# Kernel optimization log

Measured on AMD Instinct MI355X. Metric: run time of the kernel, lower is better.

The kernel has to match this reference:

```python
import jax, jax.numpy as jnp
import numpy as np

B, N, C = 8, 4096, 512

def setup_inputs() -> dict:
    key = jax.random.key(0)
    k1, k2, k3, k4, k5, k6 = jax.random.split(key, 6)
    x = jax.random.normal(k1, (B, N, C), dtype=jnp.float32)
    adj = jax.random.uniform(k2, (B, C, C), dtype=jnp.float32)
    # params: stored [in, out] so y = x @ W + b (equivalent to torch Linear)
    s = 1.0 / np.sqrt(C)
    Wqkv = jax.random.uniform(k3, (C, 3 * C), dtype=jnp.float32, minval=-s, maxval=s)
    bqkv = jax.random.uniform(k4, (3 * C,), dtype=jnp.float32, minval=-s, maxval=s)
    Wo = jax.random.uniform(k5, (C, C), dtype=jnp.float32, minval=-s, maxval=s)
    bo = jax.random.uniform(k6, (C,), dtype=jnp.float32, minval=-s, maxval=s)
    return {"x": x, "adj": adj, "Wqkv": Wqkv, "bqkv": bqkv, "Wo": Wo, "bo": bo}

def reference(x, adj, Wqkv, bqkv, Wo, bo):
    # qkv projection + ReLU gating
    qkv = jnp.einsum('bnc,cd->bnd', x, Wqkv) + bqkv          # [B,N,3C]
    q, k, v = jnp.split(qkv, 3, axis=-1)                      # each [B,N,C]
    q, k, v = jax.nn.relu(q), jax.nn.relu(k), jax.nn.relu(v)
    dk = q.shape[-1]
    # channel-wise scores: q^T k over tokens -> [B,C,C]
    scores = jnp.einsum('bnc,bnd->bcd', q, k) / jnp.sqrt(jnp.float32(dk))
    attn = jax.nn.softmax(scores, axis=-1)
    attn = attn * adj                                         # post-softmax adjacency gate
    y = jnp.einsum('bnc,bcd->bnd', v, attn)                   # value.matmul(attention)
    return jnp.einsum('bnc,cd->bnd', y, Wo) + bo
```

## Files before the change

kernel.cpp:

```cpp
#include <hip/hip_runtime.h>

#define B_ 8
#define N_ 4096
#define C_ 512

typedef _Float16 f16;
typedef __attribute__((ext_vector_type(8))) _Float16 f16x8;
typedef __attribute__((ext_vector_type(4))) _Float16 f16x4;
typedef __attribute__((ext_vector_type(4))) float f32x4;

#define GLL16(gsrc, ldst)                                                      \
  __builtin_amdgcn_global_load_lds(                                            \
      (const __attribute__((address_space(1))) void*)(gsrc),                   \
      (__attribute__((address_space(3))) void*)(ldst), 16, 0, 0)

__device__ __forceinline__ int xcd_remap(int bid, int nwg) {
  return (bid & 7) * (nwg >> 3) + (bid >> 3);
}

template <int LDA2, int LDB2, int NT>
__device__ __forceinline__ void mainloop32(const char* __restrict__ Agb,
                                           const char* __restrict__ Bgb,
                                           f16* Als, f16* Bls,
                                           f32x4 (&acc)[4][4]) {
  const int tid = threadIdx.x;
  const int lane = tid & 63;
  const int wv = tid >> 6;
  const int wr = wv >> 1;
  const int wc = wv & 1;

  const int r15 = lane & 15;
  const int g8 = (lane >> 4) << 3;
  const int swz = (r15 & 3) << 3;
  const int kx = g8 ^ swz;
  const int awbase = (wr * 64 + r15) * 32;
  const int bwbase = (wc * 64 + r15) * 32;

  int rowl[2], colb[2];
#pragma unroll
  for (int ld = 0; ld < 2; ++ld) {
    const int doff = (ld * 256 + tid) * 16;
    rowl[ld] = doff >> 6;
    colb[ld] = (doff & 63) ^ ((rowl[ld] & 3) << 4);
  }

  auto stage = [&](int t) {
    if (t >= NT) return;
    f16* la = Als + (t & 1) * 4096 + wv * 512;
    f16* lb = Bls + (t & 1) * 4096 + wv * 512;
#pragma unroll
    for (int ld = 0; ld < 2; ++ld) {
      GLL16(Agb + (size_t)rowl[ld] * LDA2 + (size_t)t * 64 + colb[ld],
            la + ld * 2048);
      GLL16(Bgb + (size_t)rowl[ld] * LDB2 + (size_t)t * 64 + colb[ld],
            lb + ld * 2048);
    }
  };

  stage(0);
  __syncthreads();

  for (int T = 0; T < NT; ++T) {
    stage(T + 1);
    const f16* Ab = Als + (T & 1) * 4096;
    const f16* Bb = Bls + (T & 1) * 4096;
    f16x8 af[4], bf[4];
#pragma unroll
    for (int m = 0; m < 4; ++m)
      af[m] = *(const f16x8*)(Ab + awbase + m * 512 + kx);
#pragma unroll
    for (int n = 0; n < 4; ++n)
      bf[n] = *(const f16x8*)(Bb + bwbase + n * 512 + kx);
#pragma unroll
    for (int m = 0; m < 4; ++m)
#pragma unroll
      for (int n = 0; n < 4; ++n)
        acc[m][n] = __builtin_amdgcn_mfma_f32_16x16x32_f16(af[m], bf[n],
                                                           acc[m][n], 0, 0, 0);
    __syncthreads();
  }
}

#define ZERO_ACC(acc)                                                          \
  f32x4 acc[4][4];                                                             \
  _Pragma("unroll") for (int zi = 0; zi < 4; ++zi)                             \
      _Pragma("unroll") for (int zj = 0; zj < 4; ++zj) {                       \
    f32x4 z = {0.f, 0.f, 0.f, 0.f};                                            \
    acc[zi][zj] = z;                                                           \
  }

__global__ void __launch_bounds__(256) k_cvt_x(const float* __restrict__ in,
                                               f16* __restrict__ out) {
  const int i = blockIdx.x * 256 + threadIdx.x;
  float4 v = ((const float4*)in)[i];
  f16x4 h = {(f16)v.x, (f16)v.y, (f16)v.z, (f16)v.w};
  ((f16x4*)out)[i] = h;
}

__global__ void __launch_bounds__(256) k_transpose_w(const float* __restrict__ w,
                                                     f16* __restrict__ wt,
                                                     int cols) {
  const int idx = blockIdx.x * 256 + threadIdx.x;
  const int n = idx >> 9;
  const int c = idx & 511;
  wt[idx] = (f16)w[(size_t)c * cols + n];
}

__global__ void __launch_bounds__(256, 4)
    k_gemm_qkv(const f16* __restrict__ x16, const f16* __restrict__ wqkvt,
               const float* __restrict__ bqkv, f16* __restrict__ q_t,
               f16* __restrict__ k_t, f16* __restrict__ v16) {
  __shared__ alignas(16) f16 Als[2 * 4096];
  __shared__ alignas(16) f16 Bls[2 * 4096];
  const int l = xcd_remap(blockIdx.x, 3072);
  const int bx = l % 12;
  const int my = l / 12;
  const char* Agb = (const char*)(x16 + (size_t)my * 128 * C_);
  const char* Bgb = (const char*)(wqkvt + (size_t)bx * 128 * C_);
  ZERO_ACC(acc);
  mainloop32<C_ * 2, C_ * 2, C_ / 32>(Agb, Bgb, Als, Bls, acc);

  const int lane = threadIdx.x & 63, wv = threadIdx.x >> 6;
  const int wr = wv >> 1, wc = wv & 1;
  const int sec = bx >> 2;
  const int colbase = bx * 128 + wc * 64;
  const int rowbase = my * 128 + wr * 64;
  const int b = rowbase >> 12;
#pragma unroll
  for (int n = 0; n < 4; ++n) {
    const int col = colbase + n * 16 + (lane & 15);
    const int cch = col & 511;
    const float bias = bqkv[col];
#pragma unroll
    for (int m = 0; m < 4; ++m) {
      const int rg = rowbase + m * 16 + ((lane >> 4) << 2);
      const int nloc = rg & 4095;
      f32x4 a = acc[m][n];
      f16x4 h = {(f16)fmaxf(a[0] + bias, 0.f), (f16)fmaxf(a[1] + bias, 0.f),
                 (f16)fmaxf(a[2] + bias, 0.f), (f16)fmaxf(a[3] + bias, 0.f)};
      if (sec == 0) {
        *(f16x4*)(q_t + ((size_t)b * C_ + cch) * N_ + nloc) = h;
      } else if (sec == 1) {
        *(f16x4*)(k_t + ((size_t)b * C_ + cch) * N_ + nloc) = h;
      } else {
        f16* dst = v16 + (size_t)rg * C_ + cch;
        dst[0] = h[0];
        dst[C_] = h[1];
        dst[2 * C_] = h[2];
        dst[3 * C_] = h[3];
      }
    }
  }
}

__global__ void __launch_bounds__(256, 4)
    k_gemm_scores(const f16* __restrict__ q_t, const f16* __restrict__ k_t,
                  f16* __restrict__ spart) {
  __shared__ alignas(16) f16 Als[2 * 4096];
  __shared__ alignas(16) f16 Bls[2 * 4096];
  const int l = xcd_remap(blockIdx.x, 1024);
  const int bx = l & 3;
  const int by = (l >> 2) & 3;
  const int z = l >> 4;
  const int b = z >> 3, sp = z & 7;
  const char* Agb = (const char*)(q_t + (size_t)b * C_ * N_ +
                                  (size_t)(by * 128) * N_ + sp * 512);
  const char* Bgb = (const char*)(k_t + (size_t)b * C_ * N_ +
                                  (size_t)(bx * 128) * N_ + sp * 512);
  ZERO_ACC(acc);
  mainloop32<N_ * 2, N_ * 2, 16>(Agb, Bgb, Als, Bls, acc);

  const int lane = threadIdx.x & 63, wv = threadIdx.x >> 6;
  const int wr = wv >> 1, wc = wv & 1;
  f16* base = spart + (size_t)(sp * B_ + b) * C_ * C_;
#pragma unroll
  for (int n = 0; n < 4; ++n) {
    const int d = bx * 128 + wc * 64 + n * 16 + (lane & 15);
#pragma unroll
    for (int m = 0; m < 4; ++m) {
      const int c0 = by * 128 + wr * 64 + m * 16 + ((lane >> 4) << 2);
#pragma unroll
      for (int r = 0; r < 4; ++r)
        base[(size_t)(c0 + r) * C_ + d] = (f16)acc[m][n][r];
    }
  }
}

__global__ void __launch_bounds__(256)
    k_softmax_gate(const f16* __restrict__ spart,
                   const float* __restrict__ adj, f16* __restrict__ attn) {
  const int wv = threadIdx.x >> 6, lane = threadIdx.x & 63;
  const int row = blockIdx.x * 4 + wv;
  const size_t ro = (size_t)row * 512;
  const int off = lane * 8;

  float s[8] = {0.f, 0.f, 0.f, 0.f, 0.f, 0.f, 0.f, 0.f};
#pragma unroll
  for (int sp = 0; sp < 8; ++sp) {
    f16x8 v = *(const f16x8*)(spart + (size_t)sp * (B_ * C_ * C_) + ro + off);
#pragma unroll
    for (int i = 0; i < 8; ++i) s[i] += (float)v[i];
  }
  const float scale = 0.044194173824159216f;
  float mx = -1e30f;
#pragma unroll
  for (int i = 0; i < 8; ++i) {
    s[i] *= scale;
    mx = fmaxf(mx, s[i]);
  }
#pragma unroll
  for (int d = 32; d > 0; d >>= 1) mx = fmaxf(mx, __shfl_xor(mx, d, 64));
  float e[8], sum = 0.f;
#pragma unroll
  for (int i = 0; i < 8; ++i) {
    e[i] = __expf(s[i] - mx);
    sum += e[i];
  }
#pragma unroll
  for (int d = 32; d > 0; d >>= 1) sum += __shfl_xor(sum, d, 64);
  const float inv = 1.0f / sum;
  const float4 a0 = *(const float4*)(adj + ro + off);
  const float4 a1 = *(const float4*)(adj + ro + off + 4);
  f16x8 o;
  o[0] = (f16)(e[0] * inv * a0.x); o[1] = (f16)(e[1] * inv * a0.y);
  o[2] = (f16)(e[2] * inv * a0.z); o[3] = (f16)(e[3] * inv * a0.w);
  o[4] = (f16)(e[4] * inv * a1.x); o[5] = (f16)(e[5] * inv * a1.y);
  o[6] = (f16)(e[6] * inv * a1.z); o[7] = (f16)(e[7] * inv * a1.w);
  *(f16x8*)(attn + ro + off) = o;
}

__global__ void __launch_bounds__(256)
    k_gemm_m(const f16* __restrict__ attn, const f16* __restrict__ wot,
             f16* __restrict__ mt) {
  __shared__ alignas(16) f16 Als[2 * 4096];
  __shared__ alignas(16) f16 Bls[2 * 4096];
  const int b = blockIdx.z;
  const char* Agb = (const char*)(attn + (size_t)b * C_ * C_ +
                                  (size_t)blockIdx.y * 128 * C_);
  const char* Bgb = (const char*)(wot + (size_t)blockIdx.x * 128 * C_);
  ZERO_ACC(acc);
  mainloop32<C_ * 2, C_ * 2, 16>(Agb, Bgb, Als, Bls, acc);

  const int lane = threadIdx.x & 63, wv = threadIdx.x >> 6;
  const int wr = wv >> 1, wc = wv & 1;
  f16* base = mt + (size_t)b * C_ * C_;
  const int colbase = blockIdx.x * 128 + wc * 64;
  const int rowbase = blockIdx.y * 128 + wr * 64;
#pragma unroll
  for (int j = 0; j < 4; ++j) {
    const int e = colbase + j * 16 + (lane & 15);
#pragma unroll
    for (int i = 0; i < 4; ++i) {
      const int c0 = rowbase + i * 16 + ((lane >> 4) << 2);
      f32x4 a = acc[i][j];
      f16x4 h = {(f16)a[0], (f16)a[1], (f16)a[2], (f16)a[3]};
      *(f16x4*)(base + (size_t)e * C_ + c0) = h;
    }
  }
}

__global__ void __launch_bounds__(256, 4)
    k_gemm_out(const f16* __restrict__ v16, const f16* __restrict__ mt,
               const float* __restrict__ bo, float* __restrict__ out) {
  __shared__ alignas(16) f16 Als[2 * 4096];
  __shared__ alignas(16) f16 Bls[2 * 4096];
  const int l = xcd_remap(blockIdx.x, 1024);
  const int bx = l & 3;
  const int my = l >> 2;
  const int b = (my * 128) >> 12;
  const char* Agb = (const char*)(v16 + (size_t)my * 128 * C_);
  const char* Bgb = (const char*)(mt + (size_t)b * C_ * C_ +
                                  (size_t)(bx * 128) * C_);
  ZERO_ACC(acc);
  mainloop32<C_ * 2, C_ * 2, 16>(Agb, Bgb, Als, Bls, acc);

  const int lane = threadIdx.x & 63, wv = threadIdx.x >> 6;
  const int wr = wv >> 1, wc = wv & 1;
#pragma unroll
  for (int n = 0; n < 4; ++n) {
    const int e = bx * 128 + wc * 64 + n * 16 + (lane & 15);
    const float bias = bo[e];
#pragma unroll
    for (int m = 0; m < 4; ++m) {
      const int rg = my * 128 + wr * 64 + m * 16 + ((lane >> 4) << 2);
#pragma unroll
      for (int r = 0; r < 4; ++r)
        out[(size_t)(rg + r) * C_ + e] = acc[m][n][r] + bias;
    }
  }
}

extern "C" void kernel_launch(void* const* d_in, const int* in_sizes, int n_in,
                              void* d_out, int out_size, void* d_ws,
                              size_t ws_size, hipStream_t stream) {
  const float* x = (const float*)d_in[0];
  const float* adj = (const float*)d_in[1];
  const float* Wqkv = (const float*)d_in[2];
  const float* bqkv = (const float*)d_in[3];
  const float* Wo = (const float*)d_in[4];
  const float* bo = (const float*)d_in[5];
  float* out = (float*)d_out;

  char* ws = (char*)d_ws;
  size_t off = 0;
  auto carve = [&](size_t bytes) -> char* {
    char* p = ws + off;
    off += (bytes + 255) & ~(size_t)255;
    return p;
  };
  f16* x16 = (f16*)carve((size_t)B_ * N_ * C_ * 2);
  f16* wqkvt = (f16*)carve((size_t)3 * C_ * C_ * 2);
  f16* wot = (f16*)carve((size_t)C_ * C_ * 2);
  f16* q_t = (f16*)carve((size_t)B_ * C_ * N_ * 2);
  f16* k_t = (f16*)carve((size_t)B_ * C_ * N_ * 2);
  f16* v16 = (f16*)carve((size_t)B_ * N_ * C_ * 2);
  f16* spart = x16;
  f16* attn16 = k_t;
  f16* mt16 = q_t;

  k_cvt_x<<<(B_ * N_ * C_ / 4) / 256, 256, 0, stream>>>(x, x16);
  k_transpose_w<<<(C_ * 3 * C_) / 256, 256, 0, stream>>>(Wqkv, wqkvt, 3 * C_);
  k_transpose_w<<<(C_ * C_) / 256, 256, 0, stream>>>(Wo, wot, C_);
  k_gemm_qkv<<<3072, 256, 0, stream>>>(x16, wqkvt, bqkv, q_t, k_t, v16);
  k_gemm_scores<<<1024, 256, 0, stream>>>(q_t, k_t, spart);
  k_softmax_gate<<<1024, 256, 0, stream>>>(spart, adj, attn16);
  k_gemm_m<<<dim3(4, 4, B_), 256, 0, stream>>>(attn16, wot, mt16);
  k_gemm_out<<<1024, 256, 0, stream>>>(v16, mt16, bo, out);
}
```

Baseline: 185.7 us.

## Fuse prep kernels, halve scores split-K, change LDS swizzle, remap gemm_m blocks

Merges the x conversion and two weight transposes into one prep launch to cut launch overhead. The scores GEMM split-K drops from 8 to 4 partitions, so there are fewer blocks with longer K loops and less partial-sum traffic for softmax to reduce. The LDS swizzle now uses row bits 1-2 instead of 0-1, aimed at reducing bank conflicts. gemm_m gets a 1D grid with XCD remapping and a launch-bounds hint. The scores GEMM now runs only 512 blocks, which may leave parts of the GPU idle.

Measured after the change: 174.3 us. 1.07x faster.

```diff
diff --git a/kernel.cpp b/kernel.cpp
--- a/kernel.cpp
+++ b/kernel.cpp
@@ -30,9 +30,9 @@
   const int wc = wv & 1;
 
   const int r15 = lane & 15;
-  const int g8 = (lane >> 4) << 3;
-  const int swz = (r15 & 3) << 3;
-  const int kx = g8 ^ swz;
+  const int kc8 = (lane >> 4) << 3;
+  const int swz = ((r15 >> 1) & 3) << 3;
+  const int kx = kc8 ^ swz;
   const int awbase = (wr * 64 + r15) * 32;
   const int bwbase = (wc * 64 + r15) * 32;
 
@@ -41,7 +41,7 @@
   for (int ld = 0; ld < 2; ++ld) {
     const int doff = (ld * 256 + tid) * 16;
     rowl[ld] = doff >> 6;
-    colb[ld] = (doff & 63) ^ ((rowl[ld] & 3) << 4);
+    colb[ld] = (doff & 63) ^ (((rowl[ld] >> 1) & 3) << 4);
   }
 
   auto stage = [&](int t) {
@@ -89,21 +89,25 @@
     acc[zi][zj] = z;                                                           \
   }
 
-__global__ void __launch_bounds__(256) k_cvt_x(const float* __restrict__ in,
-                                               f16* __restrict__ out) {
-  const int i = blockIdx.x * 256 + threadIdx.x;
-  float4 v = ((const float4*)in)[i];
-  f16x4 h = {(f16)v.x, (f16)v.y, (f16)v.z, (f16)v.w};
-  ((f16x4*)out)[i] = h;
-}
-
-__global__ void __launch_bounds__(256) k_transpose_w(const float* __restrict__ w,
-                                                     f16* __restrict__ wt,
-                                                     int cols) {
-  const int idx = blockIdx.x * 256 + threadIdx.x;
-  const int n = idx >> 9;
-  const int c = idx & 511;
-  wt[idx] = (f16)w[(size_t)c * cols + n];
+__global__ void __launch_bounds__(256)
+    k_prep(const float* __restrict__ x, const float* __restrict__ Wqkv,
+           const float* __restrict__ Wo, f16* __restrict__ x16,
+           f16* __restrict__ wqkvt, f16* __restrict__ wot) {
+  const int bid = blockIdx.x;
+  if (bid < 16384) {
+    const int i = bid * 256 + threadIdx.x;
+    float4 v = ((const float4*)x)[i];
+    f16x4 h = {(f16)v.x, (f16)v.y, (f16)v.z, (f16)v.w};
+    ((f16x4*)x16)[i] = h;
+  } else if (bid < 19456) {
+    const int idx = (bid - 16384) * 256 + threadIdx.x;
+    const int n = idx >> 9, c = idx & 511;
+    wqkvt[idx] = (f16)Wqkv[(size_t)c * 1536 + n];
+  } else {
+    const int idx = (bid - 19456) * 256 + threadIdx.x;
+    const int n = idx >> 9, c = idx & 511;
+    wot[idx] = (f16)Wo[(size_t)c * 512 + n];
+  }
 }
 
 __global__ void __launch_bounds__(256, 4)
@@ -118,7 +122,7 @@
   const char* Agb = (const char*)(x16 + (size_t)my * 128 * C_);
   const char* Bgb = (const char*)(wqkvt + (size_t)bx * 128 * C_);
   ZERO_ACC(acc);
-  mainloop32<C_ * 2, C_ * 2, C_ / 32>(Agb, Bgb, Als, Bls, acc);
+  mainloop32<C_ * 2, C_ * 2, 16>(Agb, Bgb, Als, Bls, acc);
 
   const int lane = threadIdx.x & 63, wv = threadIdx.x >> 6;
   const int wr = wv >> 1, wc = wv & 1;
@@ -158,17 +162,17 @@
                   f16* __restrict__ spart) {
   __shared__ alignas(16) f16 Als[2 * 4096];
   __shared__ alignas(16) f16 Bls[2 * 4096];
-  const int l = xcd_remap(blockIdx.x, 1024);
+  const int l = xcd_remap(blockIdx.x, 512);
   const int bx = l & 3;
   const int by = (l >> 2) & 3;
   const int z = l >> 4;
-  const int b = z >> 3, sp = z & 7;
+  const int b = z >> 2, sp = z & 3;
   const char* Agb = (const char*)(q_t + (size_t)b * C_ * N_ +
-                                  (size_t)(by * 128) * N_ + sp * 512);
+                                  (size_t)(by * 128) * N_ + sp * 1024);
   const char* Bgb = (const char*)(k_t + (size_t)b * C_ * N_ +
-                                  (size_t)(bx * 128) * N_ + sp * 512);
+                                  (size_t)(bx * 128) * N_ + sp * 1024);
   ZERO_ACC(acc);
-  mainloop32<N_ * 2, N_ * 2, 16>(Agb, Bgb, Als, Bls, acc);
+  mainloop32<N_ * 2, N_ * 2, 32>(Agb, Bgb, Als, Bls, acc);
 
   const int lane = threadIdx.x & 63, wv = threadIdx.x >> 6;
   const int wr = wv >> 1, wc = wv & 1;
@@ -196,7 +200,7 @@
 
   float s[8] = {0.f, 0.f, 0.f, 0.f, 0.f, 0.f, 0.f, 0.f};
 #pragma unroll
-  for (int sp = 0; sp < 8; ++sp) {
+  for (int sp = 0; sp < 4; ++sp) {
     f16x8 v = *(const f16x8*)(spart + (size_t)sp * (B_ * C_ * C_) + ro + off);
 #pragma unroll
     for (int i = 0; i < 8; ++i) s[i] += (float)v[i];
@@ -229,23 +233,26 @@
   *(f16x8*)(attn + ro + off) = o;
 }
 
-__global__ void __launch_bounds__(256)
+__global__ void __launch_bounds__(256, 4)
     k_gemm_m(const f16* __restrict__ attn, const f16* __restrict__ wot,
              f16* __restrict__ mt) {
   __shared__ alignas(16) f16 Als[2 * 4096];
   __shared__ alignas(16) f16 Bls[2 * 4096];
-  const int b = blockIdx.z;
+  const int l = xcd_remap(blockIdx.x, 128);
+  const int bx = l & 3;
+  const int by = (l >> 2) & 3;
+  const int b = l >> 4;
   const char* Agb = (const char*)(attn + (size_t)b * C_ * C_ +
-                                  (size_t)blockIdx.y * 128 * C_);
-  const char* Bgb = (const char*)(wot + (size_t)blockIdx.x * 128 * C_);
+                                  (size_t)(by * 128) * C_);
+  const char* Bgb = (const char*)(wot + (size_t)(bx * 128) * C_);
   ZERO_ACC(acc);
   mainloop32<C_ * 2, C_ * 2, 16>(Agb, Bgb, Als, Bls, acc);
 
   const int lane = threadIdx.x & 63, wv = threadIdx.x >> 6;
   const int wr = wv >> 1, wc = wv & 1;
   f16* base = mt + (size_t)b * C_ * C_;
-  const int colbase = blockIdx.x * 128 + wc * 64;
-  const int rowbase = blockIdx.y * 128 + wr * 64;
+  const int colbase = bx * 128 + wc * 64;
+  const int rowbase = by * 128 + wr * 64;
 #pragma unroll
   for (int j = 0; j < 4; ++j) {
     const int e = colbase + j * 16 + (lane & 15);
@@ -318,12 +325,10 @@
   f16* attn16 = k_t;
   f16* mt16 = q_t;
 
-  k_cvt_x<<<(B_ * N_ * C_ / 4) / 256, 256, 0, stream>>>(x, x16);
-  k_transpose_w<<<(C_ * 3 * C_) / 256, 256, 0, stream>>>(Wqkv, wqkvt, 3 * C_);
-  k_transpose_w<<<(C_ * C_) / 256, 256, 0, stream>>>(Wo, wot, C_);
+  k_prep<<<20480, 256, 0, stream>>>(x, Wqkv, Wo, x16, wqkvt, wot);
   k_gemm_qkv<<<3072, 256, 0, stream>>>(x16, wqkvt, bqkv, q_t, k_t, v16);
-  k_gemm_scores<<<1024, 256, 0, stream>>>(q_t, k_t, spart);
+  k_gemm_scores<<<512, 256, 0, stream>>>(q_t, k_t, spart);
   k_softmax_gate<<<1024, 256, 0, stream>>>(spart, adj, attn16);
-  k_gemm_m<<<dim3(4, 4, B_), 256, 0, stream>>>(attn16, wot, mt16);
+  k_gemm_m<<<128, 256, 0, stream>>>(attn16, wot, mt16);
   k_gemm_out<<<1024, 256, 0, stream>>>(v16, mt16, bo, out);
 }
```
